# Kernel optimization log

Hardware: AMD Instinct MI355X
Metric: run time of the kernel (lower is better)

The kernel has to match this reference:

```python
import jax, jax.numpy as jnp
import numpy as np

HIDDEN = 1024
FFN = 2048
N_EXPERTS = 8
TOP_K = 2


def setup_inputs() -> dict:
    key = jax.random.key(0)
    k_x, k_g, k1, k2, k3 = jax.random.split(key, 5)
    hidden_states = jax.random.normal(k_x, (4, 4096, HIDDEN), dtype=jnp.float32)
    gate_w = jax.random.normal(k_g, (N_EXPERTS, HIDDEN), dtype=jnp.float32) * 0.02
    # nn.Linear convention: weight is [out_features, in_features]
    w1 = jax.random.normal(k1, (N_EXPERTS, FFN, HIDDEN), dtype=jnp.float32) * 0.02
    w2 = jax.random.normal(k2, (N_EXPERTS, HIDDEN, FFN), dtype=jnp.float32) * 0.02
    w3 = jax.random.normal(k3, (N_EXPERTS, FFN, HIDDEN), dtype=jnp.float32) * 0.02
    return {"hidden_states": hidden_states, "gate_w": gate_w, "w1": w1, "w2": w2, "w3": w3}


def reference(hidden_states, gate_w, w1, w2, w3):
    B, S, H = hidden_states.shape
    E = gate_w.shape[0]
    x = hidden_states.reshape(-1, H)  # [T, H]
    T = x.shape[0]

    # Router: softmax in fp32, top-2, renormalize (matches torch reference)
    router_logits = jnp.einsum("th,eh->te", x, gate_w)
    probs = jax.nn.softmax(router_logits.astype(jnp.float32), axis=-1)
    top_w, top_i = jax.lax.top_k(probs, TOP_K)  # [T, 2]
    top_w = top_w / jnp.sum(top_w, axis=-1, keepdims=True)
    top_w = top_w.astype(x.dtype)

    # Dense combine weights [T, E]: zero for unselected experts.
    combine = jnp.zeros((T, E), dtype=x.dtype)
    combine = combine.at[jnp.arange(T)[:, None], top_i].set(top_w)

    # Per-expert SwiGLU; loop over small fixed expert count, accumulate.
    out = jnp.zeros_like(x)
    for e in range(E):
        h = jax.nn.silu(x @ w1[e].T) * (x @ w3[e].T)  # [T, FFN]
        out = out + combine[:, e:e + 1] * (h @ w2[e].T)
    return out.reshape(B, S, H)
```

## Files before the change

kernel.cpp:

```cpp
#include <hip/hip_runtime.h>
#include <cstdint>

#define H 1024
#define F 2048
#define E_N 8
#define BM 256
#define BK 64
#define NW (E_N * F * H)

typedef __attribute__((ext_vector_type(8))) short short8v;
typedef __attribute__((ext_vector_type(4))) float float4v;
typedef unsigned short u16;

__device__ __forceinline__ u16 f2bf(float f) {
    uint32_t u = __float_as_uint(f);
    u += 0x7FFFu + ((u >> 16) & 1u);
    return (u16)(u >> 16);
}
__device__ __forceinline__ float bf2f(u16 b) {
    return __uint_as_float(((uint32_t)b) << 16);
}

__device__ __forceinline__ void gload16(const void* g, void* l) {
    __builtin_amdgcn_global_load_lds((const __attribute__((address_space(1))) uint32_t*)g,
                                     (__attribute__((address_space(3))) uint32_t*)l, 16, 0, 0);
}

__device__ __forceinline__ void barx() {
    asm volatile("" ::: "memory");
    __builtin_amdgcn_s_barrier();
    asm volatile("" ::: "memory");
}

__device__ __forceinline__ void decode_swz(int bid, int nTiles, int ngy, int gyc,
                                           int& tile, int& gy) {
    int nblk = nTiles * ngy;
    int q = nblk >> 3, r = nblk & 7;
    int xcd = bid & 7, pos = bid >> 3;
    int cid = (xcd < r ? xcd * (q + 1) : r * (q + 1) + (xcd - r) * q) + pos;
    int per = nTiles * gyc;
    int chunk = cid / per, rem = cid - chunk * per;
    tile = rem / gyc;
    gy = chunk * gyc + (rem - (rem / gyc) * gyc);
}

__global__ __launch_bounds__(256) void cvt3_kernel(const float* __restrict__ s0,
                                                   const float* __restrict__ s1,
                                                   const float* __restrict__ s2,
                                                   u16* __restrict__ dst) {
    int i = (blockIdx.x * 256 + threadIdx.x) * 4;
    int stride = gridDim.x * 256 * 4;
    for (; i < 3 * NW; i += stride) {
        int seg = i / NW;
        int off = i - seg * NW;
        const float* s = (seg == 0) ? s0 : ((seg == 1) ? s1 : s2);
        float4 v = *(const float4*)(s + off);
        ushort4 o;
        o.x = f2bf(v.x); o.y = f2bf(v.y); o.z = f2bf(v.z); o.w = f2bf(v.w);
        *(ushort4*)(dst + i) = o;
    }
}

__global__ __launch_bounds__(256) void router_kernel(const float* __restrict__ x,
                                                     const float* __restrict__ gw,
                                                     int* __restrict__ topi,
                                                     float* __restrict__ topw,
                                                     u16* __restrict__ xg, int T) {
    int wave = threadIdx.x >> 6, lane = threadIdx.x & 63;
    int t = blockIdx.x * 4 + wave;
    if (t >= T) return;
    const float4* xr = (const float4*)(x + (size_t)t * H);
    float4 xv[4];
#pragma unroll
    for (int i = 0; i < 4; i++) xv[i] = xr[i * 64 + lane];
#pragma unroll
    for (int i = 0; i < 4; i++) {
        ushort4 o;
        o.x = f2bf(xv[i].x); o.y = f2bf(xv[i].y);
        o.z = f2bf(xv[i].z); o.w = f2bf(xv[i].w);
        *(ushort4*)(xg + (size_t)t * H + (i * 64 + lane) * 4) = o;
    }
    float acc[E_N];
#pragma unroll
    for (int e = 0; e < E_N; e++) {
        const float4* gr = (const float4*)(gw + e * H);
        float s = 0.f;
#pragma unroll
        for (int i = 0; i < 4; i++) {
            float4 g = gr[i * 64 + lane];
            s += xv[i].x * g.x + xv[i].y * g.y + xv[i].z * g.z + xv[i].w * g.w;
        }
        acc[e] = s;
    }
#pragma unroll
    for (int e = 0; e < E_N; e++) {
#pragma unroll
        for (int off = 32; off; off >>= 1) acc[e] += __shfl_xor(acc[e], off, 64);
    }
    if (lane == 0) {
        int i0 = 0;
#pragma unroll
        for (int e = 1; e < E_N; e++) if (acc[e] > acc[i0]) i0 = e;
        int i1 = -1;
#pragma unroll
        for (int e = 0; e < E_N; e++) {
            if (e == i0) continue;
            if (i1 < 0 || acc[e] > acc[i1]) i1 = e;
        }
        float e1 = __expf(acc[i1] - acc[i0]);
        float w0 = 1.f / (1.f + e1);
        float w1v = e1 / (1.f + e1);
        topi[t * 2] = i0; topi[t * 2 + 1] = i1;
        topw[t * 2] = w0; topw[t * 2 + 1] = w1v;
    }
}

__global__ __launch_bounds__(256) void hist_kernel(const int* __restrict__ topi,
                                                   int* __restrict__ counts, int n) {
    __shared__ int hc[E_N];
    if (threadIdx.x < E_N) hc[threadIdx.x] = 0;
    __syncthreads();
    for (int i = blockIdx.x * 256 + threadIdx.x; i < n; i += gridDim.x * 256)
        atomicAdd(&hc[topi[i]], 1);
    __syncthreads();
    if (threadIdx.x < E_N) atomicAdd(&counts[threadIdx.x], hc[threadIdx.x]);
}

__global__ void scan_kernel(const int* __restrict__ counts, int* __restrict__ offsets,
                            int* __restrict__ cursors, int* __restrict__ tileOff) {
    if (threadIdx.x == 0 && blockIdx.x == 0) {
        int o = 0, to = 0;
        for (int e = 0; e < E_N; e++) {
            offsets[e] = o; cursors[e] = o; tileOff[e] = to;
            o += counts[e];
            to += (counts[e] + BM - 1) / BM;
        }
        offsets[E_N] = o; tileOff[E_N] = to;
    }
}

__global__ __launch_bounds__(1024) void scatter_kernel(const int* __restrict__ topi,
                                                       const float* __restrict__ topw,
                                                       int* __restrict__ cursors,
                                                       int* __restrict__ perm_tok,
                                                       float* __restrict__ perm_gate,
                                                       int* __restrict__ inv, int n) {
    __shared__ int hc[E_N];
    __shared__ int base[E_N];
    int tid = threadIdx.x;
    if (tid < E_N) hc[tid] = 0;
    __syncthreads();
    int i = blockIdx.x * 1024 + tid;
    int e = 0, lrank = 0;
    bool ok = (i < n);
    if (ok) {
        e = topi[i];
        lrank = atomicAdd(&hc[e], 1);
    }
    __syncthreads();
    if (tid < E_N) base[tid] = atomicAdd(&cursors[tid], hc[tid]);
    __syncthreads();
    if (ok) {
        int pos = base[e] + lrank;
        perm_tok[pos] = i >> 1;
        perm_gate[pos] = topw[i];
        inv[i] = pos;
    }
}

__global__ __launch_bounds__(512) void stage1_kernel(
    const u16* __restrict__ xg, const u16* __restrict__ w1b, const u16* __restrict__ w3b,
    const int* __restrict__ perm_tok, const float* __restrict__ perm_gate,
    const int* __restrict__ offsets, const int* __restrict__ tileOff,
    u16* __restrict__ h, int cstart, int tpcThis) {
    __shared__ u16 lA[2 * BM * BK];
    __shared__ u16 lB1[2 * 128 * BK];
    __shared__ u16 lB3[2 * 128 * BK];
    __shared__ int ptokS[BM];
    __shared__ float pgateS[BM];

    int tileL, nbIdx;
    decode_swz(blockIdx.x, tpcThis, F / 128, 4, tileL, nbIdx);
    int tile = cstart + tileL;
    if (tile >= tileOff[E_N]) return;
    int e = 0;
    while (e < E_N - 1 && tile >= tileOff[e + 1]) e++;
    int rbase = offsets[e] + (tile - tileOff[e]) * BM;
    int segEnd = offsets[e + 1];
    int e0 = 0;
    while (e0 < E_N - 1 && cstart >= tileOff[e0 + 1]) e0++;
    int chunkBase = offsets[e0] + (cstart - tileOff[e0]) * BM;

    int tid = threadIdx.x;
    if (tid < BM) {
        int p = rbase + tid; if (p > segEnd - 1) p = segEnd - 1;
        ptokS[tid] = perm_tok[p];
        pgateS[tid] = perm_gate[p];
    }
    __syncthreads();

    int lane = tid & 63, wid = tid >> 6;
    int wr = wid >> 2, wc = wid & 3;
    int lrow = lane & 15, kgrp = lane >> 4;
    int lr = lane >> 3, csw = ((lane & 7) ^ lr) << 3;
    int nb = nbIdx * 128;
    const u16* w1p = w1b + (size_t)e * F * H + (size_t)nb * H;
    const u16* w3p = w3b + (size_t)e * F * H + (size_t)nb * H;

    const u16* pA[4];
#pragma unroll
    for (int j = 0; j < 4; j++) pA[j] = xg + (size_t)ptokS[(j * 8 + wid) * 8 + lr] * H + csw;
    const u16 *pB1[2], *pB3[2];
#pragma unroll
    for (int j = 0; j < 2; j++) {
        int rr = (j * 8 + wid) * 8 + lr;
        pB1[j] = w1p + (size_t)rr * H + csw;
        pB3[j] = w3p + (size_t)rr * H + csw;
    }

    int swe0 = (kgrp ^ (lrow & 7)) << 3;
    int swe1 = ((4 + kgrp) ^ (lrow & 7)) << 3;
    int eA0 = (wr * 128 + lrow) * BK + swe0;
    int eA1 = (wr * 128 + lrow) * BK + swe1;
    int eB0 = (wc * 32 + lrow) * BK + swe0;
    int eB1 = (wc * 32 + lrow) * BK + swe1;

#define STA(CC, j)  gload16(pA[j],  &lA[(CC) * 16384 + ((j) * 8 + wid) * 8 * BK])
#define STB1(CC, j) gload16(pB1[j], &lB1[(CC) * 8192 + ((j) * 8 + wid) * 8 * BK])
#define STB3(CC, j) gload16(pB3[j], &lB3[(CC) * 8192 + ((j) * 8 + wid) * 8 * BK])

    float4v acc1[8][2], acc3[8][2];
#pragma unroll
    for (int a = 0; a < 8; a++)
#pragma unroll
        for (int b = 0; b < 2; b++) { acc1[a][b] = (float4v)(0.f); acc3[a][b] = (float4v)(0.f); }

    STB1(0, 0); STB1(0, 1);
    STB3(0, 0); STB3(0, 1);
    STA(0, 0); STA(0, 2); STA(0, 1); STA(0, 3);
#pragma unroll
    for (int j = 0; j < 4; j++) pA[j] += BK;
    pB1[0] += BK; pB1[1] += BK; pB3[0] += BK; pB3[1] += BK;
    asm volatile("s_waitcnt vmcnt(2)" ::: "memory");
    barx();

#define S1_DSA(CC, p) \
    short8v aF[2][2]; \
    _Pragma("unroll") \
    for (int pm = 0; pm < 2; pm++) { \
        aF[pm][0] = *(const short8v*)&lA[eA0 + (CC) * 16384 + (2 * (p) + pm) * 1024]; \
        aF[pm][1] = *(const short8v*)&lA[eA1 + (CC) * 16384 + (2 * (p) + pm) * 1024]; \
    }
#define S1_MM(p) \
    __builtin_amdgcn_s_setprio(1); \
    _Pragma("unroll") \
    for (int pm = 0; pm < 2; pm++) \
    _Pragma("unroll") \
    for (int n = 0; n < 2; n++) \
    _Pragma("unroll") \
    for (int kk = 0; kk < 2; kk++) { \
        acc1[2 * (p) + pm][n] = __builtin_amdgcn_mfma_f32_16x16x32_bf16(aF[pm][kk], b1F[n][kk], acc1[2 * (p) + pm][n], 0, 0, 0); \
        acc3[2 * (p) + pm][n] = __builtin_amdgcn_mfma_f32_16x16x32_bf16(aF[pm][kk], b3F[n][kk], acc3[2 * (p) + pm][n], 0, 0, 0); \
    } \
    __builtin_amdgcn_s_setprio(0);

#define S1_KT(CC, LAST) { \
    short8v b1F[2][2], b3F[2][2]; \
    _Pragma("unroll") \
    for (int n = 0; n < 2; n++) { \
        b1F[n][0] = *(const short8v*)&lB1[eB0 + (CC) * 8192 + n * 1024]; \
        b1F[n][1] = *(const short8v*)&lB1[eB1 + (CC) * 8192 + n * 1024]; \
        b3F[n][0] = *(const short8v*)&lB3[eB0 + (CC) * 8192 + n * 1024]; \
        b3F[n][1] = *(const short8v*)&lB3[eB1 + (CC) * 8192 + n * 1024]; \
    } \
    { S1_DSA(CC, 0) \
      if (!(LAST)) { STB1((CC) ^ 1, 0); STB1((CC) ^ 1, 1); STA((CC) ^ 1, 0); } \
      S1_MM(0) } \
    { S1_DSA(CC, 1) \
      if (!(LAST)) { STB3((CC) ^ 1, 0); STB3((CC) ^ 1, 1); STA((CC) ^ 1, 2); } \
      S1_MM(1) } \
    if (!(LAST)) { asm volatile("s_waitcnt vmcnt(6)" ::: "memory"); } \
    else         { asm volatile("s_waitcnt vmcnt(0)" ::: "memory"); } \
    barx(); \
    { S1_DSA(CC, 2) \
      if (!(LAST)) { STA((CC) ^ 1, 1); } \
      S1_MM(2) } \
    { S1_DSA(CC, 3) \
      if (!(LAST)) { STA((CC) ^ 1, 3); } \
      S1_MM(3) } \
    if (!(LAST)) { asm volatile("s_waitcnt vmcnt(2)" ::: "memory"); } \
    else         { asm volatile("s_waitcnt vmcnt(0)" ::: "memory"); } \
    barx(); \
    _Pragma("unroll") \
    for (int j = 0; j < 4; j++) pA[j] += BK; \
    pB1[0] += BK; pB1[1] += BK; pB3[0] += BK; pB3[1] += BK; \
}

    for (int tt = 0; tt < (H / BK) - 2; tt += 2) {
        S1_KT(0, false)
        S1_KT(1, false)
    }
    S1_KT(0, false)
    S1_KT(1, true)
#undef S1_DSA
#undef S1_MM
#undef S1_KT
#undef STA
#undef STB1
#undef STB3

    int rif = (lane >> 4) * 4;
#pragma unroll
    for (int m = 0; m < 8; m++) {
#pragma unroll
        for (int reg = 0; reg < 4; reg++) {
            int rowIdx = wr * 128 + m * 16 + rif + reg;
            int p = rbase + rowIdx;
            if (p < segEnd) {
                float g = pgateS[rowIdx];
#pragma unroll
                for (int n = 0; n < 2; n++) {
                    float a1 = acc1[m][n][reg], a3 = acc3[m][n][reg];
                    float sv = a1 / (1.f + __expf(-a1));
                    float hv = sv * a3 * g;
                    int ncol = nb + wc * 32 + n * 16 + (lane & 15);
                    h[(size_t)(p - chunkBase) * F + ncol] = f2bf(hv);
                }
            }
        }
    }
}

template<int NREP>
__global__ __launch_bounds__(512) void stage2_kernel(
    const u16* __restrict__ h, const u16* __restrict__ w2b,
    const int* __restrict__ offsets, const int* __restrict__ tileOff,
    u16* __restrict__ y, int cstart, int tpcThis) {
    constexpr int BN = NREP * 64;
    constexpr int BSTRIDE = BN * BK;
    __shared__ u16 lA[2 * BM * BK];
    __shared__ u16 lB[2 * BSTRIDE];

    int tileL, nbIdx;
    decode_swz(blockIdx.x, tpcThis, H / BN, 4, tileL, nbIdx);
    int tile = cstart + tileL;
    if (tile >= tileOff[E_N]) return;
    int e = 0;
    while (e < E_N - 1 && tile >= tileOff[e + 1]) e++;
    int rbase = offsets[e] + (tile - tileOff[e]) * BM;
    int segEnd = offsets[e + 1];
    int e0 = 0;
    while (e0 < E_N - 1 && cstart >= tileOff[e0 + 1]) e0++;
    int chunkBase = offsets[e0] + (cstart - tileOff[e0]) * BM;

    int tid = threadIdx.x;
    int lane = tid & 63, wid = tid >> 6;
    int wr = wid >> 2, wc = wid & 3;
    int lrow = lane & 15, kgrp = lane >> 4;
    int lr = lane >> 3, csw = ((lane & 7) ^ lr) << 3;
    int nb = nbIdx * BN;
    const u16* w2p = w2b + (size_t)e * H * F + (size_t)nb * F;

    const u16* pA[4];
#pragma unroll
    for (int j = 0; j < 4; j++) {
        int rb = (j * 8 + wid) * 8;
        int p = rbase + rb + lr; if (p > segEnd - 1) p = segEnd - 1;
        pA[j] = h + (size_t)(p - chunkBase) * F + csw;
    }
    const u16* pB[NREP];
#pragma unroll
    for (int j = 0; j < NREP; j++) pB[j] = w2p + (size_t)((j * 8 + wid) * 8 + lr) * F + csw;

    int swe0 = (kgrp ^ (lrow & 7)) << 3;
    int swe1 = ((4 + kgrp) ^ (lrow & 7)) << 3;
    int eA0 = (wr * 128 + lrow) * BK + swe0;
    int eA1 = (wr * 128 + lrow) * BK + swe1;
    int eB0 = (wc * (NREP * 16) + lrow) * BK + swe0;
    int eB1 = (wc * (NREP * 16) + lrow) * BK + swe1;

#define STA2(CC, j) gload16(pA[j], &lA[(CC) * 16384 + ((j) * 8 + wid) * 8 * BK])
#define STB2(CC, j) gload16(pB[j], &lB[(CC) * BSTRIDE + ((j) * 8 + wid) * 8 * BK])

    float4v acc[8][NREP];
#pragma unroll
    for (int a = 0; a < 8; a++)
#pragma unroll
        for (int b = 0; b < NREP; b++) acc[a][b] = (float4v)(0.f);

#pragma unroll
    for (int j = 0; j < NREP; j++) STB2(0, j);
    STA2(0, 0); STA2(0, 2); STA2(0, 1); STA2(0, 3);
#pragma unroll
    for (int j = 0; j < 4; j++) pA[j] += BK;
#pragma unroll
    for (int j = 0; j < NREP; j++) pB[j] += BK;
    asm volatile("s_waitcnt vmcnt(2)" ::: "memory");
    barx();

#define S2_DSA(CC, p) \
    short8v aF[2][2]; \
    _Pragma("unroll") \
    for (int pm = 0; pm < 2; pm++) { \
        aF[pm][0] = *(const short8v*)&lA[eA0 + (CC) * 16384 + (2 * (p) + pm) * 1024]; \
        aF[pm][1] = *(const short8v*)&lA[eA1 + (CC) * 16384 + (2 * (p) + pm) * 1024]; \
    }
#define S2_MM(p) \
    __builtin_amdgcn_s_setprio(1); \
    _Pragma("unroll") \
    for (int pm = 0; pm < 2; pm++) \
    _Pragma("unroll") \
    for (int n = 0; n < NREP; n++) \
    _Pragma("unroll") \
    for (int kk = 0; kk < 2; kk++) \
        acc[2 * (p) + pm][n] = __builtin_amdgcn_mfma_f32_16x16x32_bf16(aF[pm][kk], bF[n][kk], acc[2 * (p) + pm][n], 0, 0, 0); \
    __builtin_amdgcn_s_setprio(0);

#define S2_KT(CC, LAST) { \
    short8v bF[NREP][2]; \
    _Pragma("unroll") \
    for (int n = 0; n < NREP; n++) { \
        bF[n][0] = *(const short8v*)&lB[eB0 + (CC) * BSTRIDE + n * 1024]; \
        bF[n][1] = *(const short8v*)&lB[eB1 + (CC) * BSTRIDE + n * 1024]; \
    } \
    { S2_DSA(CC, 0) \
      if (!(LAST)) { STB2((CC) ^ 1, 0); if (NREP == 4) STB2((CC) ^ 1, 1); STA2((CC) ^ 1, 0); } \
      S2_MM(0) } \
    { S2_DSA(CC, 1) \
      if (!(LAST)) { if (NREP == 4) { STB2((CC) ^ 1, 2); STB2((CC) ^ 1, 3); } else STB2((CC) ^ 1, 1); \
                     STA2((CC) ^ 1, 2); } \
      S2_MM(1) } \
    if (!(LAST)) { \
        if (NREP == 4) { asm volatile("s_waitcnt vmcnt(6)" ::: "memory"); } \
        else           { asm volatile("s_waitcnt vmcnt(4)" ::: "memory"); } \
    } else { asm volatile("s_waitcnt vmcnt(0)" ::: "memory"); } \
    barx(); \
    { S2_DSA(CC, 2) \
      if (!(LAST)) { STA2((CC) ^ 1, 1); } \
      S2_MM(2) } \
    { S2_DSA(CC, 3) \
      if (!(LAST)) { STA2((CC) ^ 1, 3); } \
      S2_MM(3) } \
    if (!(LAST)) { asm volatile("s_waitcnt vmcnt(2)" ::: "memory"); } \
    else         { asm volatile("s_waitcnt vmcnt(0)" ::: "memory"); } \
    barx(); \
    _Pragma("unroll") \
    for (int j = 0; j < 4; j++) pA[j] += BK; \
    _Pragma("unroll") \
    for (int j = 0; j < NREP; j++) pB[j] += BK; \
}

    for (int tt = 0; tt < (F / BK) - 2; tt += 2) {
        S2_KT(0, false)
        S2_KT(1, false)
    }
    S2_KT(0, false)
    S2_KT(1, true)
#undef S2_DSA
#undef S2_MM
#undef S2_KT
#undef STA2
#undef STB2

    int rif = (lane >> 4) * 4;
#pragma unroll
    for (int m = 0; m < 8; m++) {
#pragma unroll
        for (int reg = 0; reg < 4; reg++) {
            int rowIdx = wr * 128 + m * 16 + rif + reg;
            int p = rbase + rowIdx;
            if (p < segEnd) {
#pragma unroll
                for (int n = 0; n < NREP; n++) {
                    int col = nb + wc * (BN / 4) + n * 16 + (lane & 15);
                    y[(size_t)p * H + col] = f2bf(acc[m][n][reg]);
                }
            }
        }
    }
}

__global__ __launch_bounds__(256) void combine_kernel(const u16* __restrict__ y,
                                                      const int* __restrict__ inv,
                                                      float* __restrict__ out) {
    int t = blockIdx.x, c = threadIdx.x;
    int s0 = inv[t * 2], s1 = inv[t * 2 + 1];
    ushort4 a = *(const ushort4*)(y + (size_t)s0 * H + c * 4);
    ushort4 b = *(const ushort4*)(y + (size_t)s1 * H + c * 4);
    float4 o;
    o.x = bf2f(a.x) + bf2f(b.x);
    o.y = bf2f(a.y) + bf2f(b.y);
    o.z = bf2f(a.z) + bf2f(b.z);
    o.w = bf2f(a.w) + bf2f(b.w);
    *(float4*)(out + (size_t)t * H + c * 4) = o;
}

extern "C" void kernel_launch(void* const* d_in, const int* in_sizes, int n_in,
                              void* d_out, int out_size, void* d_ws, size_t ws_size,
                              hipStream_t stream) {
    (void)n_in; (void)out_size;
    const float* x  = (const float*)d_in[0];
    const float* gw = (const float*)d_in[1];
    const float* w1 = (const float*)d_in[2];
    const float* w2 = (const float*)d_in[3];
    const float* w3 = (const float*)d_in[4];
    float* out = (float*)d_out;
    int T = in_sizes[0] / H;
    int P = T * 2;

    char* ws = (char*)d_ws;
    size_t off = 0;
    auto alloc = [&](size_t b) { size_t c = off; off = (off + b + 255) & ~(size_t)255; return c; };
    size_t misc_o  = alloc(256);
    int* counts  = (int*)(ws + misc_o);
    int* offsets = (int*)(ws + misc_o + 64);
    int* cursors = (int*)(ws + misc_o + 128);
    int* tileOff = (int*)(ws + misc_o + 192);
    size_t topi_o  = alloc((size_t)T * 2 * 4);
    size_t topw_o  = alloc((size_t)T * 2 * 4);
    size_t ptok_o  = alloc((size_t)P * 4);
    size_t pgate_o = alloc((size_t)P * 4);
    size_t inv_o   = alloc((size_t)T * 2 * 4);
    size_t wb_o  = alloc((size_t)3 * NW * 2);
    size_t xg_o  = alloc((size_t)T * H * 2);
    size_t y_o   = alloc((size_t)P * H * 2);
    u16* w1b = (u16*)(ws + wb_o);
    u16* w3b = w1b + NW;
    u16* w2b = w1b + 2 * (size_t)NW;

    int maxTiles = P / BM + E_N;
    size_t perTile = (size_t)BM * F * 2;
    size_t avail = (ws_size > off + 256) ? (ws_size - off - 256) : 0;
    int tpc = (int)(avail / perTile);
    if (tpc > maxTiles) tpc = maxTiles;
    if (tpc < 4) tpc = 4;
    size_t h_o = alloc((size_t)tpc * perTile);

    hipMemsetAsync(ws + misc_o, 0, 256, stream);

    cvt3_kernel<<<8192, 256, 0, stream>>>(w1, w3, w2, w1b);
    router_kernel<<<T / 4, 256, 0, stream>>>(x, gw, (int*)(ws + topi_o), (float*)(ws + topw_o),
                                             (u16*)(ws + xg_o), T);
    hist_kernel<<<32, 256, 0, stream>>>((int*)(ws + topi_o), counts, P);
    scan_kernel<<<1, 64, 0, stream>>>(counts, offsets, cursors, tileOff);
    scatter_kernel<<<(P + 1023) / 1024, 1024, 0, stream>>>(
        (int*)(ws + topi_o), (float*)(ws + topw_o), cursors,
        (int*)(ws + ptok_o), (float*)(ws + pgate_o), (int*)(ws + inv_o), P);

    for (int cstart = 0; cstart < maxTiles; cstart += tpc) {
        int tpcThis = maxTiles - cstart; if (tpcThis > tpc) tpcThis = tpc;
        stage1_kernel<<<tpcThis * (F / 128), 512, 0, stream>>>(
            (u16*)(ws + xg_o), w1b, w3b,
            (int*)(ws + ptok_o), (float*)(ws + pgate_o), offsets, tileOff,
            (u16*)(ws + h_o), cstart, tpcThis);
        if (tpcThis * 4 >= 240)
            stage2_kernel<4><<<tpcThis * (H / 256), 512, 0, stream>>>(
                (u16*)(ws + h_o), w2b, offsets, tileOff,
                (u16*)(ws + y_o), cstart, tpcThis);
        else
            stage2_kernel<2><<<tpcThis * (H / 128), 512, 0, stream>>>(
                (u16*)(ws + h_o), w2b, offsets, tileOff,
                (u16*)(ws + y_o), cstart, tpcThis);
    }
    combine_kernel<<<T, 256, 0, stream>>>((u16*)(ws + y_o), (int*)(ws + inv_o), out);
}
```

Baseline: 609.8 us.

## Load weight B fragments directly from global into registers, bypassing LDS

Both GEMM stages stop staging the expert weight tiles (w1/w3 and w2) through shared memory. Each wave now loads its own MFMA B fragments straight from global memory into double-buffered registers, and the vmcnt wait counts are adjusted to match. This is meant to remove LDS traffic, LDS capacity use and ds_read pressure for B. In exchange, each wave issues its own uncoalesced 16-byte row loads, weight data shared across waves is fetched redundantly, and register pressure rises.

```diff
diff --git a/kernel.cpp b/kernel.cpp
--- a/kernel.cpp
+++ b/kernel.cpp
@@ -174,8 +174,6 @@
     const int* __restrict__ offsets, const int* __restrict__ tileOff,
     u16* __restrict__ h, int cstart, int tpcThis) {
     __shared__ u16 lA[2 * BM * BK];
-    __shared__ u16 lB1[2 * 128 * BK];
-    __shared__ u16 lB3[2 * 128 * BK];
     __shared__ int ptokS[BM];
     __shared__ float pgateS[BM];
 
@@ -210,37 +208,46 @@
     const u16* pA[4];
 #pragma unroll
     for (int j = 0; j < 4; j++) pA[j] = xg + (size_t)ptokS[(j * 8 + wid) * 8 + lr] * H + csw;
-    const u16 *pB1[2], *pB3[2];
-#pragma unroll
-    for (int j = 0; j < 2; j++) {
-        int rr = (j * 8 + wid) * 8 + lr;
-        pB1[j] = w1p + (size_t)rr * H + csw;
-        pB3[j] = w3p + (size_t)rr * H + csw;
+
+    const u16 *pB1g[2], *pB3g[2];
+#pragma unroll
+    for (int n = 0; n < 2; n++) {
+        int bcol = wc * 32 + n * 16 + lrow;
+        pB1g[n] = w1p + (size_t)bcol * H + kgrp * 8;
+        pB3g[n] = w3p + (size_t)bcol * H + kgrp * 8;
     }
 
     int swe0 = (kgrp ^ (lrow & 7)) << 3;
     int swe1 = ((4 + kgrp) ^ (lrow & 7)) << 3;
     int eA0 = (wr * 128 + lrow) * BK + swe0;
     int eA1 = (wr * 128 + lrow) * BK + swe1;
-    int eB0 = (wc * 32 + lrow) * BK + swe0;
-    int eB1 = (wc * 32 + lrow) * BK + swe1;
 
 #define STA(CC, j)  gload16(pA[j],  &lA[(CC) * 16384 + ((j) * 8 + wid) * 8 * BK])
-#define STB1(CC, j) gload16(pB1[j], &lB1[(CC) * 8192 + ((j) * 8 + wid) * 8 * BK])
-#define STB3(CC, j) gload16(pB3[j], &lB3[(CC) * 8192 + ((j) * 8 + wid) * 8 * BK])
-
+#define LDB1(CC) \
+    _Pragma("unroll") \
+    for (int n = 0; n < 2; n++) { \
+        b1R[CC][n][0] = *(const short8v*)(pB1g[n]); \
+        b1R[CC][n][1] = *(const short8v*)(pB1g[n] + 32); \
+    }
+#define LDB3(CC) \
+    _Pragma("unroll") \
+    for (int n = 0; n < 2; n++) { \
+        b3R[CC][n][0] = *(const short8v*)(pB3g[n]); \
+        b3R[CC][n][1] = *(const short8v*)(pB3g[n] + 32); \
+    }
+
+    short8v b1R[2][2][2], b3R[2][2][2];
     float4v acc1[8][2], acc3[8][2];
 #pragma unroll
     for (int a = 0; a < 8; a++)
 #pragma unroll
         for (int b = 0; b < 2; b++) { acc1[a][b] = (float4v)(0.f); acc3[a][b] = (float4v)(0.f); }
 
-    STB1(0, 0); STB1(0, 1);
-    STB3(0, 0); STB3(0, 1);
+    LDB1(0) LDB3(0)
     STA(0, 0); STA(0, 2); STA(0, 1); STA(0, 3);
 #pragma unroll
     for (int j = 0; j < 4; j++) pA[j] += BK;
-    pB1[0] += BK; pB1[1] += BK; pB3[0] += BK; pB3[1] += BK;
+    pB1g[0] += BK; pB1g[1] += BK; pB3g[0] += BK; pB3g[1] += BK;
     asm volatile("s_waitcnt vmcnt(2)" ::: "memory");
     barx();
 
@@ -251,7 +258,7 @@
         aF[pm][0] = *(const short8v*)&lA[eA0 + (CC) * 16384 + (2 * (p) + pm) * 1024]; \
         aF[pm][1] = *(const short8v*)&lA[eA1 + (CC) * 16384 + (2 * (p) + pm) * 1024]; \
     }
-#define S1_MM(p) \
+#define S1_MM(CC, p) \
     __builtin_amdgcn_s_setprio(1); \
     _Pragma("unroll") \
     for (int pm = 0; pm < 2; pm++) \
@@ -259,41 +266,33 @@
     for (int n = 0; n < 2; n++) \
     _Pragma("unroll") \
     for (int kk = 0; kk < 2; kk++) { \
-        acc1[2 * (p) + pm][n] = __builtin_amdgcn_mfma_f32_16x16x32_bf16(aF[pm][kk], b1F[n][kk], acc1[2 * (p) + pm][n], 0, 0, 0); \
-        acc3[2 * (p) + pm][n] = __builtin_amdgcn_mfma_f32_16x16x32_bf16(aF[pm][kk], b3F[n][kk], acc3[2 * (p) + pm][n], 0, 0, 0); \
+        acc1[2 * (p) + pm][n] = __builtin_amdgcn_mfma_f32_16x16x32_bf16(aF[pm][kk], b1R[CC][n][kk], acc1[2 * (p) + pm][n], 0, 0, 0); \
+        acc3[2 * (p) + pm][n] = __builtin_amdgcn_mfma_f32_16x16x32_bf16(aF[pm][kk], b3R[CC][n][kk], acc3[2 * (p) + pm][n], 0, 0, 0); \
     } \
     __builtin_amdgcn_s_setprio(0);
 
 #define S1_KT(CC, LAST) { \
-    short8v b1F[2][2], b3F[2][2]; \
-    _Pragma("unroll") \
-    for (int n = 0; n < 2; n++) { \
-        b1F[n][0] = *(const short8v*)&lB1[eB0 + (CC) * 8192 + n * 1024]; \
-        b1F[n][1] = *(const short8v*)&lB1[eB1 + (CC) * 8192 + n * 1024]; \
-        b3F[n][0] = *(const short8v*)&lB3[eB0 + (CC) * 8192 + n * 1024]; \
-        b3F[n][1] = *(const short8v*)&lB3[eB1 + (CC) * 8192 + n * 1024]; \
-    } \
     { S1_DSA(CC, 0) \
-      if (!(LAST)) { STB1((CC) ^ 1, 0); STB1((CC) ^ 1, 1); STA((CC) ^ 1, 0); } \
-      S1_MM(0) } \
+      if (!(LAST)) { LDB1((CC) ^ 1) STA((CC) ^ 1, 0); } \
+      S1_MM(CC, 0) } \
     { S1_DSA(CC, 1) \
-      if (!(LAST)) { STB3((CC) ^ 1, 0); STB3((CC) ^ 1, 1); STA((CC) ^ 1, 2); } \
-      S1_MM(1) } \
-    if (!(LAST)) { asm volatile("s_waitcnt vmcnt(6)" ::: "memory"); } \
+      if (!(LAST)) { LDB3((CC) ^ 1) STA((CC) ^ 1, 2); } \
+      S1_MM(CC, 1) } \
+    if (!(LAST)) { asm volatile("s_waitcnt vmcnt(10)" ::: "memory"); } \
     else         { asm volatile("s_waitcnt vmcnt(0)" ::: "memory"); } \
     barx(); \
     { S1_DSA(CC, 2) \
       if (!(LAST)) { STA((CC) ^ 1, 1); } \
-      S1_MM(2) } \
+      S1_MM(CC, 2) } \
     { S1_DSA(CC, 3) \
       if (!(LAST)) { STA((CC) ^ 1, 3); } \
-      S1_MM(3) } \
+      S1_MM(CC, 3) } \
     if (!(LAST)) { asm volatile("s_waitcnt vmcnt(2)" ::: "memory"); } \
     else         { asm volatile("s_waitcnt vmcnt(0)" ::: "memory"); } \
     barx(); \
     _Pragma("unroll") \
     for (int j = 0; j < 4; j++) pA[j] += BK; \
-    pB1[0] += BK; pB1[1] += BK; pB3[0] += BK; pB3[1] += BK; \
+    pB1g[0] += BK; pB1g[1] += BK; pB3g[0] += BK; pB3g[1] += BK; \
 }
 
     for (int tt = 0; tt < (H / BK) - 2; tt += 2) {
@@ -306,8 +305,8 @@
 #undef S1_MM
 #undef S1_KT
 #undef STA
-#undef STB1
-#undef STB3
+#undef LDB1
+#undef LDB3
 
     int rif = (lane >> 4) * 4;
 #pragma unroll
@@ -337,9 +336,7 @@
     const int* __restrict__ offsets, const int* __restrict__ tileOff,
     u16* __restrict__ y, int cstart, int tpcThis) {
     constexpr int BN = NREP * 64;
-    constexpr int BSTRIDE = BN * BK;
     __shared__ u16 lA[2 * BM * BK];
-    __shared__ u16 lB[2 * BSTRIDE];
 
     int tileL, nbIdx;
     decode_swz(blockIdx.x, tpcThis, H / BN, 4, tileL, nbIdx);
@@ -368,33 +365,43 @@
         int p = rbase + rb + lr; if (p > segEnd - 1) p = segEnd - 1;
         pA[j] = h + (size_t)(p - chunkBase) * F + csw;
     }
-    const u16* pB[NREP];
-#pragma unroll
-    for (int j = 0; j < NREP; j++) pB[j] = w2p + (size_t)((j * 8 + wid) * 8 + lr) * F + csw;
+    const u16* pBg[NREP];
+#pragma unroll
+    for (int n = 0; n < NREP; n++)
+        pBg[n] = w2p + (size_t)(wc * (NREP * 16) + n * 16 + lrow) * F + kgrp * 8;
 
     int swe0 = (kgrp ^ (lrow & 7)) << 3;
     int swe1 = ((4 + kgrp) ^ (lrow & 7)) << 3;
     int eA0 = (wr * 128 + lrow) * BK + swe0;
     int eA1 = (wr * 128 + lrow) * BK + swe1;
-    int eB0 = (wc * (NREP * 16) + lrow) * BK + swe0;
-    int eB1 = (wc * (NREP * 16) + lrow) * BK + swe1;
 
 #define STA2(CC, j) gload16(pA[j], &lA[(CC) * 16384 + ((j) * 8 + wid) * 8 * BK])
-#define STB2(CC, j) gload16(pB[j], &lB[(CC) * BSTRIDE + ((j) * 8 + wid) * 8 * BK])
-
+#define LDB2A(CC) \
+    _Pragma("unroll") \
+    for (int n = 0; n < NREP / 2; n++) { \
+        bR[CC][n][0] = *(const short8v*)(pBg[n]); \
+        bR[CC][n][1] = *(const short8v*)(pBg[n] + 32); \
+    }
+#define LDB2B(CC) \
+    _Pragma("unroll") \
+    for (int n = NREP / 2; n < NREP; n++) { \
+        bR[CC][n][0] = *(const short8v*)(pBg[n]); \
+        bR[CC][n][1] = *(const short8v*)(pBg[n] + 32); \
+    }
+
+    short8v bR[2][NREP][2];
     float4v acc[8][NREP];
 #pragma unroll
     for (int a = 0; a < 8; a++)
 #pragma unroll
         for (int b = 0; b < NREP; b++) acc[a][b] = (float4v)(0.f);
 
-#pragma unroll
-    for (int j = 0; j < NREP; j++) STB2(0, j);
+    LDB2A(0) LDB2B(0)
     STA2(0, 0); STA2(0, 2); STA2(0, 1); STA2(0, 3);
 #pragma unroll
     for (int j = 0; j < 4; j++) pA[j] += BK;
 #pragma unroll
-    for (int j = 0; j < NREP; j++) pB[j] += BK;
+    for (int n = 0; n < NREP; n++) pBg[n] += BK;
     asm volatile("s_waitcnt vmcnt(2)" ::: "memory");
     barx();
 
@@ -405,7 +412,7 @@
         aF[pm][0] = *(const short8v*)&lA[eA0 + (CC) * 16384 + (2 * (p) + pm) * 1024]; \
         aF[pm][1] = *(const short8v*)&lA[eA1 + (CC) * 16384 + (2 * (p) + pm) * 1024]; \
     }
-#define S2_MM(p) \
+#define S2_MM(CC, p) \
     __builtin_amdgcn_s_setprio(1); \
     _Pragma("unroll") \
     for (int pm = 0; pm < 2; pm++) \
@@ -413,41 +420,34 @@
     for (int n = 0; n < NREP; n++) \
     _Pragma("unroll") \
     for (int kk = 0; kk < 2; kk++) \
-        acc[2 * (p) + pm][n] = __builtin_amdgcn_mfma_f32_16x16x32_bf16(aF[pm][kk], bF[n][kk], acc[2 * (p) + pm][n], 0, 0, 0); \
+        acc[2 * (p) + pm][n] = __builtin_amdgcn_mfma_f32_16x16x32_bf16(aF[pm][kk], bR[CC][n][kk], acc[2 * (p) + pm][n], 0, 0, 0); \
     __builtin_amdgcn_s_setprio(0);
 
 #define S2_KT(CC, LAST) { \
-    short8v bF[NREP][2]; \
-    _Pragma("unroll") \
-    for (int n = 0; n < NREP; n++) { \
-        bF[n][0] = *(const short8v*)&lB[eB0 + (CC) * BSTRIDE + n * 1024]; \
-        bF[n][1] = *(const short8v*)&lB[eB1 + (CC) * BSTRIDE + n * 1024]; \
-    } \
     { S2_DSA(CC, 0) \
-      if (!(LAST)) { STB2((CC) ^ 1, 0); if (NREP == 4) STB2((CC) ^ 1, 1); STA2((CC) ^ 1, 0); } \
-      S2_MM(0) } \
+      if (!(LAST)) { LDB2A((CC) ^ 1) STA2((CC) ^ 1, 0); } \
+      S2_MM(CC, 0) } \
     { S2_DSA(CC, 1) \
-      if (!(LAST)) { if (NREP == 4) { STB2((CC) ^ 1, 2); STB2((CC) ^ 1, 3); } else STB2((CC) ^ 1, 1); \
-                     STA2((CC) ^ 1, 2); } \
-      S2_MM(1) } \
+      if (!(LAST)) { LDB2B((CC) ^ 1) STA2((CC) ^ 1, 2); } \
+      S2_MM(CC, 1) } \
     if (!(LAST)) { \
-        if (NREP == 4) { asm volatile("s_waitcnt vmcnt(6)" ::: "memory"); } \
-        else           { asm volatile("s_waitcnt vmcnt(4)" ::: "memory"); } \
+        if (NREP == 4) { asm volatile("s_waitcnt vmcnt(10)" ::: "memory"); } \
+        else           { asm volatile("s_waitcnt vmcnt(6)" ::: "memory"); } \
     } else { asm volatile("s_waitcnt vmcnt(0)" ::: "memory"); } \
     barx(); \
     { S2_DSA(CC, 2) \
       if (!(LAST)) { STA2((CC) ^ 1, 1); } \
-      S2_MM(2) } \
+      S2_MM(CC, 2) } \
     { S2_DSA(CC, 3) \
       if (!(LAST)) { STA2((CC) ^ 1, 3); } \
-      S2_MM(3) } \
+      S2_MM(CC, 3) } \
     if (!(LAST)) { asm volatile("s_waitcnt vmcnt(2)" ::: "memory"); } \
     else         { asm volatile("s_waitcnt vmcnt(0)" ::: "memory"); } \
     barx(); \
     _Pragma("unroll") \
     for (int j = 0; j < 4; j++) pA[j] += BK; \
     _Pragma("unroll") \
-    for (int j = 0; j < NREP; j++) pB[j] += BK; \
+    for (int n = 0; n < NREP; n++) pBg[n] += BK; \
 }
 
     for (int tt = 0; tt < (F / BK) - 2; tt += 2) {
@@ -460,7 +460,8 @@
 #undef S2_MM
 #undef S2_KT
 #undef STA2
-#undef STB2
+#undef LDB2A
+#undef LDB2B
 
     int rif = (lane >> 4) * 4;
 #pragma unroll
```

Measured after the change: 785.3 us. 28.8% more time.
